# Kernel tuning notes

Hardware: AMD Instinct MI355X
Metric: run time of the kernel (lower is better)

Reference implementation:

```python
import jax, jax.numpy as jnp
import numpy as np

B, N, C = 2048, 4096, 1024
UNITS, RANK = 4096, 512


def _orth(key, shape):
    a = jax.random.normal(key, shape, dtype=jnp.float32)
    q, r = jnp.linalg.qr(a if shape[0] >= shape[1] else a.T)
    q = q * jnp.sign(jnp.diagonal(r))[None, :]
    return q if shape[0] >= shape[1] else q.T


def setup_inputs() -> dict:
    key = jax.random.key(0)
    k1, k2, k3, k4, k5, k6 = jax.random.split(key, 6)
    inputs = jax.random.normal(k1, (B, N), dtype=jnp.float32)
    context = jax.random.normal(k2, (B, C), dtype=jnp.float32)
    U = _orth(k3, (N, RANK))
    V = _orth(k4, (UNITS, RANK))
    W = _orth(k5, (C, RANK))
    # SingularValueInitializer stand-in: positive values scaled like glorot singular values
    S = jnp.abs(jax.random.normal(k6, (RANK,), dtype=jnp.float32)) * jnp.sqrt(2.0 / (N + UNITS))
    bias = jnp.zeros((UNITS,), dtype=jnp.float32)
    return {"inputs": inputs, "context": context, "U": U, "S": S, "V": V, "W": W, "bias": bias}


def reference(inputs, context, U, S, V, W, bias):
    # s_b = S + context @ W  -> per-batch singular values [B, R]
    s = S[None, :] + context @ W
    # Original: kernel_b = U diag(s_b) V^T; out_b = x_b @ kernel_b.
    # Associativity: out = ((x @ U) * s) @ V^T  -- identical math, no [B,N,M] intermediate.
    xu = inputs @ U                      # [B, R]
    out = (xu * s) @ V.T                 # [B, UNITS]
    out = out + bias[None, :]
    return jax.nn.relu(out)
```

## Files before the change

### kernel.cpp

```cpp
#include <hip/hip_runtime.h>
#include <hip/hip_bf16.h>

typedef __attribute__((ext_vector_type(8))) __bf16 bf16x8;
typedef __attribute__((ext_vector_type(4))) float f32x4;
typedef __attribute__((ext_vector_type(8))) unsigned short ushort8;
typedef __attribute__((ext_vector_type(4))) unsigned short ushort4v;

__device__ __forceinline__ unsigned short f2bf(float f) {
  unsigned u = __builtin_bit_cast(unsigned, f);
  u += 0x7FFFu + ((u >> 16) & 1u);
  return (unsigned short)(u >> 16);
}

__device__ __forceinline__ void gload_lds16(const void* g, void* l) {
  __builtin_amdgcn_global_load_lds(
      (const __attribute__((address_space(1))) void*)g,
      (__attribute__((address_space(3))) void*)l, 16, 0, 0);
}

__device__ __forceinline__ void barrier_fence() {
  __builtin_amdgcn_s_barrier();
  asm volatile("" ::: "memory");
}

template <int N>
__device__ __forceinline__ void waitvm() {
  if constexpr (N == 0)      asm volatile("s_waitcnt vmcnt(0)" ::: "memory");
  else if constexpr (N == 6) asm volatile("s_waitcnt vmcnt(6)" ::: "memory");
  else if constexpr (N == 8) asm volatile("s_waitcnt vmcnt(8)" ::: "memory");
}

__global__ __launch_bounds__(256) void prep_kernel(
    const float* __restrict__ U, unsigned short* __restrict__ Ut,
    const float* __restrict__ W, unsigned short* __restrict__ Wt,
    const float* __restrict__ V, unsigned short* __restrict__ Vb) {
  __shared__ float tile[32][33];
  const int b = blockIdx.x;
  const int tid = threadIdx.x;
  if (b < 2560) {
    const float* src;
    unsigned short* dst;
    int rows, cols, bx, by;
    if (b < 2048) {
      src = U; dst = Ut; rows = 4096; cols = 512;
      bx = (b & 15) * 32; by = (b >> 4) * 32;
    } else {
      int bb = b - 2048;
      src = W; dst = Wt; rows = 1024; cols = 512;
      bx = (bb & 15) * 32; by = (bb >> 4) * 32;
    }
    const int tx = tid & 31, ty = tid >> 5;
    for (int i = ty; i < 32; i += 8)
      tile[i][tx] = src[(size_t)(by + i) * cols + bx + tx];
    __syncthreads();
    for (int i = ty; i < 32; i += 8)
      dst[(size_t)(bx + i) * rows + by + tx] = f2bf(tile[tx][i]);
  } else {
    const size_t i = (size_t)(b - 2560) * 256 + tid;
    const float4* s4 = reinterpret_cast<const float4*>(V) + 2 * i;
    float4 a = s4[0], c = s4[1];
    ushort8 o;
    o[0] = f2bf(a.x); o[1] = f2bf(a.y); o[2] = f2bf(a.z); o[3] = f2bf(a.w);
    o[4] = f2bf(c.x); o[5] = f2bf(c.y); o[6] = f2bf(c.z); o[7] = f2bf(c.w);
    *(reinterpret_cast<ushort8*>(Vb) + i) = o;
  }
}

template <int EPI, bool AF32>
__device__ __forceinline__ void gemm_core(
    const void* __restrict__ Av, const unsigned short* __restrict__ Bt,
    int N, int lda, int kchunk, int k0, const float* __restrict__ e0,
    float* __restrict__ outf, int nwg, int bid) {
  constexpr int FM = 2, FN = 4;
  constexpr int BM = 32 * FM, BN = 32 * FN, BK = 64;
  constexpr int ABYTES = BM * BK * (AF32 ? 4 : 2);
  constexpr int AI = AF32 ? 4 : 2;
  constexpr int BI = 4;
  constexpr int ISS = AI + BI;
  __shared__ __align__(16) char lds[2][ABYTES + BN * BK * 2];

  const int tid = threadIdx.x;
  const int wid = tid >> 6;
  const int lane = tid & 63;
  const int wr = wid >> 1, wc = wid & 1;

  const int swz = (bid & 7) * (nwg >> 3) + (bid >> 3);
  const int nbn = N / BN;
  const int brow = (swz / nbn) * BM;
  const int bcol = (swz % nbn) * BN;

  f32x4 zero = {0.f, 0.f, 0.f, 0.f};
  f32x4 acc[FM][FN];
#pragma unroll
  for (int m = 0; m < FM; ++m)
#pragma unroll
    for (int n = 0; n < FN; ++n) acc[m][n] = zero;

  const int lr = lane >> 3;
  const int swzc = ((lane & 7) ^ lr) * 8;
  const int a4r = lane >> 4;
  const int a4c = lane & 15;
  const int colE = ((a4c ^ a4r) << 2);
  const int colO = ((a4c ^ (4 + a4r)) << 2);

  const float* Agf =
      (const float*)Av + (size_t)(brow + wid * 16 + a4r) * lda + k0;
  const unsigned short* Agh =
      (const unsigned short*)Av + (size_t)(brow + wid * 16 + lr) * lda + swzc + k0;
  const unsigned short* Bgh = Bt + (size_t)(bcol + wid * 32 + lr) * lda + swzc + k0;

  const int frow = lane & 15;
  const int fhi = lane >> 4;

  const int nsteps = kchunk / BK;

  auto stage = [&](int b, int kofs) {
    char* dstA = lds[b] + wid * (AF32 ? 4096 : 2048);
    if constexpr (AF32) {
#pragma unroll
      for (int i = 0; i < 4; ++i)
        gload_lds16(Agf + kofs + (size_t)(4 * i) * lda + ((i & 1) ? colO : colE),
                    dstA + i * 1024);
    } else {
#pragma unroll
      for (int i = 0; i < 2; ++i)
        gload_lds16(Agh + kofs + (size_t)(8 * i) * lda, dstA + i * 1024);
    }
    char* dstB = lds[b] + ABYTES + wid * 4096;
#pragma unroll
    for (int i = 0; i < BI; ++i)
      gload_lds16(Bgh + kofs + (size_t)(8 * i) * lda, dstB + i * 1024);
  };

  auto compute = [&](int cur) {
    const char* base = lds[cur];
    const unsigned short* Bs = (const unsigned short*)(base + ABYTES);
#pragma unroll
    for (int ks = 0; ks < 2; ++ks) {
      bf16x8 af[FM], bg[FN];
#pragma unroll
      for (int m = 0; m < FM; ++m) {
        int row = wr * FM * 16 + m * 16 + frow;
        int j = ks * 4 + fhi;
        if constexpr (AF32) {
          const float* ap = (const float*)base + row * 64;
          int r7 = row & 7;
          float4 lo = *(const float4*)(ap + (((2 * j) ^ r7) << 2));
          float4 hi = *(const float4*)(ap + (((2 * j + 1) ^ r7) << 2));
          bf16x8 tv;
          tv[0] = (__bf16)lo.x; tv[1] = (__bf16)lo.y;
          tv[2] = (__bf16)lo.z; tv[3] = (__bf16)lo.w;
          tv[4] = (__bf16)hi.x; tv[5] = (__bf16)hi.y;
          tv[6] = (__bf16)hi.z; tv[7] = (__bf16)hi.w;
          af[m] = tv;
        } else {
          int pc = j ^ (row & 7);
          af[m] = *(const bf16x8*)((const unsigned short*)base + row * 64 + pc * 8);
        }
      }
#pragma unroll
      for (int n = 0; n < FN; ++n) {
        int row = wc * FN * 16 + n * 16 + frow;
        int pc = (ks * 4 + fhi) ^ (row & 7);
        bg[n] = *(const bf16x8*)(Bs + row * 64 + pc * 8);
      }
#pragma unroll
      for (int m = 0; m < FM; ++m)
#pragma unroll
        for (int n = 0; n < FN; ++n)
          acc[m][n] = __builtin_amdgcn_mfma_f32_16x16x32_bf16(af[m], bg[n],
                                                              acc[m][n], 0, 0, 0);
    }
  };

  stage(0, 0);
  stage(1, BK);

  int cur = 0;
  for (int t = 0; t < nsteps; ++t) {
    if (t + 1 < nsteps)
      waitvm<ISS>();
    else
      waitvm<0>();
    barrier_fence();
    compute(cur);
    if (t + 1 < nsteps) {
      asm volatile("s_waitcnt lgkmcnt(0)" ::: "memory");
      barrier_fence();
      if (t + 2 < nsteps) stage(cur, (t + 2) * BK);
    }
    cur ^= 1;
  }

#pragma unroll
  for (int m = 0; m < FM; ++m) {
    int gr0 = brow + wr * FM * 16 + m * 16 + fhi * 4;
#pragma unroll
    for (int n = 0; n < FN; ++n) {
      int gc = bcol + wc * FN * 16 + n * 16 + frow;
#pragma unroll
      for (int j = 0; j < 4; ++j) {
        size_t idx = (size_t)(gr0 + j) * N + gc;
        float v = acc[m][n][j];
        if constexpr (EPI == 2) {
          v += e0[gc];
          outf[idx] = v > 0.f ? v : 0.f;
        } else {
          outf[idx] = v;
        }
      }
    }
  }
}

__global__ __launch_bounds__(256) void gemm01_kernel(
    const float* __restrict__ inp, const unsigned short* __restrict__ Ut,
    const float* __restrict__ ctx, const unsigned short* __restrict__ Wt,
    float* __restrict__ p0, float* __restrict__ p1) {
  const int bid = (int)blockIdx.x;
  constexpr size_t MN = (size_t)2048 * 512;
  if (bid < 512) {
    const int split = bid >> 7;
    gemm_core<3, true>(inp, Ut, 512, 4096, 1024, split * 1024, nullptr,
                       p1 + split * MN, 128, bid & 127);
  } else {
    const int sb = bid - 512;
    const int split = sb >> 7;
    gemm_core<3, true>(ctx, Wt, 512, 1024, 512, split * 512, nullptr,
                       p0 + split * MN, 128, sb & 127);
  }
}

__global__ __launch_bounds__(256) void gemm2_kernel(
    const unsigned short* __restrict__ xus, const unsigned short* __restrict__ Vb,
    const float* __restrict__ bias, float* __restrict__ out) {
  gemm_core<2, false>(xus, Vb, 4096, 512, 512, 0, bias, out, 1024,
                      (int)blockIdx.x);
}

__global__ void reduce_mul_kernel(const float* __restrict__ p1,
                                  const float* __restrict__ p0,
                                  const float* __restrict__ Svec,
                                  unsigned short* __restrict__ xus, int MN) {
  int i = blockIdx.x * blockDim.x + threadIdx.x;
  size_t base = (size_t)i * 4;
  if (base >= (size_t)MN) return;
  float4 a = *reinterpret_cast<const float4*>(p1 + base);
  float4 b = *reinterpret_cast<const float4*>(p1 + (size_t)MN + base);
  float4 c = *reinterpret_cast<const float4*>(p1 + 2 * (size_t)MN + base);
  float4 d = *reinterpret_cast<const float4*>(p1 + 3 * (size_t)MN + base);
  float4 s0 = *reinterpret_cast<const float4*>(p0 + base);
  float4 s1 = *reinterpret_cast<const float4*>(p0 + (size_t)MN + base);
  float4 sv = *reinterpret_cast<const float4*>(Svec + (base & 511));
  float4 xu, s;
  xu.x = (a.x + b.x) + (c.x + d.x);  s.x = s0.x + s1.x + sv.x;
  xu.y = (a.y + b.y) + (c.y + d.y);  s.y = s0.y + s1.y + sv.y;
  xu.z = (a.z + b.z) + (c.z + d.z);  s.z = s0.z + s1.z + sv.z;
  xu.w = (a.w + b.w) + (c.w + d.w);  s.w = s0.w + s1.w + sv.w;
  ushort4v o;
  o[0] = f2bf(xu.x * s.x);
  o[1] = f2bf(xu.y * s.y);
  o[2] = f2bf(xu.z * s.z);
  o[3] = f2bf(xu.w * s.w);
  *reinterpret_cast<ushort4v*>(xus + base) = o;
}

extern "C" void kernel_launch(void* const* d_in, const int* in_sizes, int n_in,
                              void* d_out, int out_size, void* d_ws, size_t ws_size,
                              hipStream_t stream) {
  constexpr int Bm = 2048, Nn = 4096, Cc = 1024, UU = 4096, RR = 512;
  const float* inputs  = (const float*)d_in[0];
  const float* context = (const float*)d_in[1];
  const float* U       = (const float*)d_in[2];
  const float* S       = (const float*)d_in[3];
  const float* V       = (const float*)d_in[4];
  const float* W       = (const float*)d_in[5];
  const float* bias    = (const float*)d_in[6];
  float* out = (float*)d_out;

  char* p = (char*)d_ws;
  unsigned short* Ut   = (unsigned short*)p; p += (size_t)RR * Nn * 2;
  unsigned short* Wt   = (unsigned short*)p; p += (size_t)RR * Cc * 2;
  unsigned short* Vb   = (unsigned short*)p; p += (size_t)UU * RR * 2;
  float*          p0   = (float*)p;          p += (size_t)2 * Bm * RR * 4;
  float*          p1   = (float*)p;          p += (size_t)4 * Bm * RR * 4;
  unsigned short* xus  = (unsigned short*)p; p += (size_t)Bm * RR * 2;

  prep_kernel<<<3584, 256, 0, stream>>>(U, Ut, W, Wt, V, Vb);

  gemm01_kernel<<<768, 256, 0, stream>>>(inputs, Ut, context, Wt, p0, p1);

  reduce_mul_kernel<<<Bm * RR / 4 / 256, 256, 0, stream>>>(p1, p0, S, xus, Bm * RR);

  gemm2_kernel<<<1024, 256, 0, stream>>>(xus, Vb, bias, out);
}
```

Before: 58.25 us.

## Drop split-K partials, fuse scale epilogue into xU GEMM, column-major tile map

Replaces the split-K GEMMs and the separate reduce/multiply pass with two full-K GEMMs. The first computes s = S + context@W with the bias folded into its epilogue. The second computes x@U with 64x64 tiles and multiplies by s in its epilogue, writing bf16 directly. This removes the fp32 partial buffers, their round trip through memory and one launch, but cuts parallelism to 128 and 256 workgroups with long K loops and serializes the s GEMM ahead of the xU GEMM. The output GEMM also switches to a column-major tile ordering to change cache reuse of V.

```diff
diff --git a/kernel.cpp b/kernel.cpp
--- a/kernel.cpp
+++ b/kernel.cpp
@@ -4,7 +4,6 @@
 typedef __attribute__((ext_vector_type(8))) __bf16 bf16x8;
 typedef __attribute__((ext_vector_type(4))) float f32x4;
 typedef __attribute__((ext_vector_type(8))) unsigned short ushort8;
-typedef __attribute__((ext_vector_type(4))) unsigned short ushort4v;
 
 __device__ __forceinline__ unsigned short f2bf(float f) {
   unsigned u = __builtin_bit_cast(unsigned, f);
@@ -66,16 +65,17 @@
   }
 }
 
-template <int EPI, bool AF32>
+template <int FM, int FN, int EPI, bool AF32, bool COLMAP>
 __device__ __forceinline__ void gemm_core(
     const void* __restrict__ Av, const unsigned short* __restrict__ Bt,
-    int N, int lda, int kchunk, int k0, const float* __restrict__ e0,
-    float* __restrict__ outf, int nwg, int bid) {
-  constexpr int FM = 2, FN = 4;
+    int N, int lda, int kchunk, const float* __restrict__ e0,
+    float* __restrict__ outf, unsigned short* __restrict__ outb,
+    int nwg, int bid) {
+  static_assert(FM == 2, "A staging geometry assumes BM=64");
   constexpr int BM = 32 * FM, BN = 32 * FN, BK = 64;
   constexpr int ABYTES = BM * BK * (AF32 ? 4 : 2);
   constexpr int AI = AF32 ? 4 : 2;
-  constexpr int BI = 4;
+  constexpr int BI = BN / 32;
   constexpr int ISS = AI + BI;
   __shared__ __align__(16) char lds[2][ABYTES + BN * BK * 2];
 
@@ -86,8 +86,15 @@
 
   const int swz = (bid & 7) * (nwg >> 3) + (bid >> 3);
   const int nbn = N / BN;
-  const int brow = (swz / nbn) * BM;
-  const int bcol = (swz % nbn) * BN;
+  int brow, bcol;
+  if constexpr (COLMAP) {
+    const int nbm = nwg / nbn;
+    brow = (swz % nbm) * BM;
+    bcol = (swz / nbm) * BN;
+  } else {
+    brow = (swz / nbn) * BM;
+    bcol = (swz % nbn) * BN;
+  }
 
   f32x4 zero = {0.f, 0.f, 0.f, 0.f};
   f32x4 acc[FM][FN];
@@ -104,10 +111,11 @@
   const int colO = ((a4c ^ (4 + a4r)) << 2);
 
   const float* Agf =
-      (const float*)Av + (size_t)(brow + wid * 16 + a4r) * lda + k0;
+      (const float*)Av + (size_t)(brow + wid * 16 + a4r) * lda;
   const unsigned short* Agh =
-      (const unsigned short*)Av + (size_t)(brow + wid * 16 + lr) * lda + swzc + k0;
-  const unsigned short* Bgh = Bt + (size_t)(bcol + wid * 32 + lr) * lda + swzc + k0;
+      (const unsigned short*)Av + (size_t)(brow + wid * 16 + lr) * lda + swzc;
+  const unsigned short* Bgh =
+      Bt + (size_t)(bcol + wid * (BN / 4) + lr) * lda + swzc;
 
   const int frow = lane & 15;
   const int fhi = lane >> 4;
@@ -126,7 +134,7 @@
       for (int i = 0; i < 2; ++i)
         gload_lds16(Agh + kofs + (size_t)(8 * i) * lda, dstA + i * 1024);
     }
-    char* dstB = lds[b] + ABYTES + wid * 4096;
+    char* dstB = lds[b] + ABYTES + wid * (BN * 32);
 #pragma unroll
     for (int i = 0; i < BI; ++i)
       gload_lds16(Bgh + kofs + (size_t)(8 * i) * lda, dstB + i * 1024);
@@ -202,67 +210,38 @@
       for (int j = 0; j < 4; ++j) {
         size_t idx = (size_t)(gr0 + j) * N + gc;
         float v = acc[m][n][j];
-        if constexpr (EPI == 2) {
+        if constexpr (EPI == 0) {
+          outf[idx] = v + e0[gc];
+        } else if constexpr (EPI == 1) {
+          outb[idx] = f2bf(v * e0[idx]);
+        } else {
           v += e0[gc];
           outf[idx] = v > 0.f ? v : 0.f;
-        } else {
-          outf[idx] = v;
         }
       }
     }
   }
 }
 
-__global__ __launch_bounds__(256) void gemm01_kernel(
+__global__ __launch_bounds__(256) void sgemm_kernel(
+    const float* __restrict__ ctx, const unsigned short* __restrict__ Wt,
+    const float* __restrict__ S, float* __restrict__ sbuf) {
+  gemm_core<2, 4, 0, true, false>(ctx, Wt, 512, 1024, 1024, S, sbuf, nullptr,
+                                  128, (int)blockIdx.x);
+}
+
+__global__ __launch_bounds__(256) void gemm1_kernel(
     const float* __restrict__ inp, const unsigned short* __restrict__ Ut,
-    const float* __restrict__ ctx, const unsigned short* __restrict__ Wt,
-    float* __restrict__ p0, float* __restrict__ p1) {
-  const int bid = (int)blockIdx.x;
-  constexpr size_t MN = (size_t)2048 * 512;
-  if (bid < 512) {
-    const int split = bid >> 7;
-    gemm_core<3, true>(inp, Ut, 512, 4096, 1024, split * 1024, nullptr,
-                       p1 + split * MN, 128, bid & 127);
-  } else {
-    const int sb = bid - 512;
-    const int split = sb >> 7;
-    gemm_core<3, true>(ctx, Wt, 512, 1024, 512, split * 512, nullptr,
-                       p0 + split * MN, 128, sb & 127);
-  }
+    const float* __restrict__ sbuf, unsigned short* __restrict__ xus) {
+  gemm_core<2, 2, 1, true, false>(inp, Ut, 512, 4096, 4096, sbuf, nullptr, xus,
+                                  256, (int)blockIdx.x);
 }
 
 __global__ __launch_bounds__(256) void gemm2_kernel(
     const unsigned short* __restrict__ xus, const unsigned short* __restrict__ Vb,
     const float* __restrict__ bias, float* __restrict__ out) {
-  gemm_core<2, false>(xus, Vb, 4096, 512, 512, 0, bias, out, 1024,
-                      (int)blockIdx.x);
-}
-
-__global__ void reduce_mul_kernel(const float* __restrict__ p1,
-                                  const float* __restrict__ p0,
-                                  const float* __restrict__ Svec,
-                                  unsigned short* __restrict__ xus, int MN) {
-  int i = blockIdx.x * blockDim.x + threadIdx.x;
-  size_t base = (size_t)i * 4;
-  if (base >= (size_t)MN) return;
-  float4 a = *reinterpret_cast<const float4*>(p1 + base);
-  float4 b = *reinterpret_cast<const float4*>(p1 + (size_t)MN + base);
-  float4 c = *reinterpret_cast<const float4*>(p1 + 2 * (size_t)MN + base);
-  float4 d = *reinterpret_cast<const float4*>(p1 + 3 * (size_t)MN + base);
-  float4 s0 = *reinterpret_cast<const float4*>(p0 + base);
-  float4 s1 = *reinterpret_cast<const float4*>(p0 + (size_t)MN + base);
-  float4 sv = *reinterpret_cast<const float4*>(Svec + (base & 511));
-  float4 xu, s;
-  xu.x = (a.x + b.x) + (c.x + d.x);  s.x = s0.x + s1.x + sv.x;
-  xu.y = (a.y + b.y) + (c.y + d.y);  s.y = s0.y + s1.y + sv.y;
-  xu.z = (a.z + b.z) + (c.z + d.z);  s.z = s0.z + s1.z + sv.z;
-  xu.w = (a.w + b.w) + (c.w + d.w);  s.w = s0.w + s1.w + sv.w;
-  ushort4v o;
-  o[0] = f2bf(xu.x * s.x);
-  o[1] = f2bf(xu.y * s.y);
-  o[2] = f2bf(xu.z * s.z);
-  o[3] = f2bf(xu.w * s.w);
-  *reinterpret_cast<ushort4v*>(xus + base) = o;
+  gemm_core<2, 4, 2, false, true>(xus, Vb, 4096, 512, 512, bias, out, nullptr,
+                                  1024, (int)blockIdx.x);
 }
 
 extern "C" void kernel_launch(void* const* d_in, const int* in_sizes, int n_in,
@@ -282,15 +261,14 @@
   unsigned short* Ut   = (unsigned short*)p; p += (size_t)RR * Nn * 2;
   unsigned short* Wt   = (unsigned short*)p; p += (size_t)RR * Cc * 2;
   unsigned short* Vb   = (unsigned short*)p; p += (size_t)UU * RR * 2;
-  float*          p0   = (float*)p;          p += (size_t)2 * Bm * RR * 4;
-  float*          p1   = (float*)p;          p += (size_t)4 * Bm * RR * 4;
+  float*          sbuf = (float*)p;          p += (size_t)Bm * RR * 4;
   unsigned short* xus  = (unsigned short*)p; p += (size_t)Bm * RR * 2;
 
   prep_kernel<<<3584, 256, 0, stream>>>(U, Ut, W, Wt, V, Vb);
 
-  gemm01_kernel<<<768, 256, 0, stream>>>(inputs, Ut, context, Wt, p0, p1);
-
-  reduce_mul_kernel<<<Bm * RR / 4 / 256, 256, 0, stream>>>(p1, p0, S, xus, Bm * RR);
+  sgemm_kernel<<<128, 256, 0, stream>>>(context, Wt, S, sbuf);
+
+  gemm1_kernel<<<256, 256, 0, stream>>>(inputs, Ut, sbuf, xus);
 
   gemm2_kernel<<<1024, 256, 0, stream>>>(xus, Vb, bias, out);
 }
```

Result: slower. 72.02 us (+23.7%).
